# Kernel tuning notes

Hardware: AMD Instinct MI355X
Metric: run time of the kernel (lower is better)

Reference implementation:

```python
import jax, jax.numpy as jnp
import numpy as np

THRESHOLD = 0.35
NEGPOS = 7
VAR0, VAR1 = 0.1, 0.2


def point_form(boxes):
    # (cx,cy,w,h) -> (x1,y1,x2,y2)
    return jnp.concatenate([boxes[:, :2] - boxes[:, 2:] / 2,
                            boxes[:, :2] + boxes[:, 2:] / 2], axis=1)


def jaccard(box_a, box_b):
    # box_a: [T,4], box_b: [P,4] in point form -> IoU [T,P]
    max_xy = jnp.minimum(box_a[:, None, 2:], box_b[None, :, 2:])
    min_xy = jnp.maximum(box_a[:, None, :2], box_b[None, :, :2])
    wh = jnp.clip(max_xy - min_xy, 0.0)
    inter = wh[..., 0] * wh[..., 1]
    area_a = ((box_a[:, 2] - box_a[:, 0]) * (box_a[:, 3] - box_a[:, 1]))[:, None]
    area_b = ((box_b[:, 2] - box_b[:, 0]) * (box_b[:, 3] - box_b[:, 1]))[None, :]
    return inter / (area_a + area_b - inter)


def encode(matched, priors):
    # matched: [P,4] point form, priors: [P,4] center form
    g_cxcy = ((matched[:, :2] + matched[:, 2:]) / 2 - priors[:, :2]) / (VAR0 * priors[:, 2:])
    g_wh = jnp.log((matched[:, 2:] - matched[:, :2]) / priors[:, 2:]) / VAR1
    return jnp.concatenate([g_cxcy, g_wh], axis=1)


def encode_landm(matched, priors):
    m = matched.reshape(-1, 5, 2)                       # [P,5,2]
    g = (m - priors[:, None, :2]) / (VAR0 * priors[:, None, 2:])
    return g.reshape(-1, 10)


def match_one(truths, labels, landms, priors):
    # truths [T,4], labels [T], landms [T,10], priors [P,4]
    overlaps = jaccard(truths, point_form(priors))       # [T,P]
    best_prior_idx = jnp.argmax(overlaps, axis=1)        # [T]
    best_truth_overlap = overlaps.max(axis=0)            # [P]
    best_truth_idx = jnp.argmax(overlaps, axis=0)        # [P]
    best_truth_overlap = best_truth_overlap.at[best_prior_idx].set(2.0)
    def body(j, bti):
        return bti.at[best_prior_idx[j]].set(j)
    best_truth_idx = jax.lax.fori_loop(0, truths.shape[0], body, best_truth_idx)
    conf = jnp.where(best_truth_overlap < THRESHOLD, 0.0, labels[best_truth_idx])
    loc = encode(truths[best_truth_idx], priors)
    landm = encode_landm(landms[best_truth_idx], priors)
    return loc, conf, landm


def smooth_l1(p, t):
    d = jnp.abs(p - t)
    return jnp.where(d < 1.0, 0.5 * d * d, d - 0.5)


def reference(loc_data, conf_data, landm_data, priors, targets):
    num, num_priors, _ = loc_data.shape
    truths = targets[:, :, :4]
    landms = targets[:, :, 4:14]
    labels = targets[:, :, 14]
    loc_t, conf_f, landm_t = jax.vmap(match_one, in_axes=(0, 0, 0, None))(
        truths, labels, landms, priors)
    conf_t = conf_f.astype(jnp.int32)                    # [num, P]

    poslands = conf_t > 0
    loss_landm = jnp.sum(smooth_l1(landm_data, landm_t) * poslands[..., None])

    pos = conf_t != 0
    loss_l = jnp.sum(smooth_l1(loc_data, loc_t) * pos[..., None])

    conf_t = jnp.where(pos, 1, conf_t)
    # per-prior CE: logsumexp - logit[target]
    ce = jax.nn.logsumexp(conf_data, axis=-1) - \
        jnp.take_along_axis(conf_data, conf_t[..., None], axis=-1)[..., 0]

    # hard negative mining: rank negatives by CE, keep top negpos*num_pos
    loss_rank = jnp.where(pos, 0.0, ce)
    loss_idx = jnp.argsort(-loss_rank, axis=1)
    idx_rank = jnp.argsort(loss_idx, axis=1)
    num_pos = pos.sum(axis=1)
    num_neg = jnp.clip(NEGPOS * num_pos, 0, num_priors - 1)
    neg = idx_rank < num_neg[:, None]

    sel = pos | neg
    loss_c = jnp.sum(ce * sel)

    N = jnp.maximum(num_pos.sum().astype(loc_data.dtype), 1.0)
    N1 = jnp.maximum(poslands.sum().astype(loc_data.dtype), 1.0)
    return loss_l / N, loss_c / N, loss_landm / N1


def setup_inputs() -> dict:
    key = jax.random.key(0)
    ks = jax.random.split(key, 8)
    N, T, P = 16, 48, 65536
    loc_data = jax.random.normal(ks[0], (N, P, 4), dtype=jnp.float32) * 0.1
    conf_data = jax.random.normal(ks[1], (N, P, 2), dtype=jnp.float32)
    landm_data = jax.random.normal(ks[2], (N, P, 10), dtype=jnp.float32) * 0.1
    # priors in (cx,cy,w,h), w,h > 0
    pc = jax.random.uniform(ks[3], (P, 2), minval=0.05, maxval=0.95)
    pwh = jax.random.uniform(ks[4], (P, 2), minval=0.04, maxval=0.3)
    priors = jnp.concatenate([pc, pwh], axis=1).astype(jnp.float32)
    # GT boxes: valid point-form (x1<x2, y1<y2)
    tc = jax.random.uniform(ks[5], (N, T, 2), minval=0.1, maxval=0.9)
    twh = jax.random.uniform(ks[6], (N, T, 2), minval=0.05, maxval=0.3)
    boxes = jnp.concatenate([tc - twh / 2, tc + twh / 2], axis=-1)
    lm = jax.random.uniform(ks[7], (N, T, 10))
    labels = jnp.ones((N, T, 1))
    targets = jnp.concatenate([boxes, lm, labels], axis=-1).astype(jnp.float32)
    return {"loc_data": loc_data, "conf_data": conf_data,
            "landm_data": landm_data, "priors": priors, "targets": targets}
```

## Files before the change

kernel.cpp:

```cpp
#include <hip/hip_runtime.h>

#define NP 65536
#define NT 48
#define TH 0.35f
#define PPT 2
#define KC_BX 128
#define NCHUNK 16
#define NCPY 4

#define PERCHUNK_OFF 0
#define HISTC_OFF    98304
#define HISTS_OFF    622592
#define NEGSUM_OFF   1146880
#define PART_OFF     1147136
#define HIST_DWORDS  262144

__device__ __forceinline__ float sml1(float d) {
    float a = fabsf(d);
    return a < 1.f ? 0.5f * a * a : a - 0.5f;
}

__global__ __launch_bounds__(256) void kA(const float* __restrict__ priors,
                                          const float* __restrict__ targets,
                                          unsigned long long* __restrict__ perchunk,
                                          unsigned int* __restrict__ histz) {
    const int chunk = blockIdx.x, tg = blockIdx.y, b = blockIdx.z;
    {
        int flat = (b * 6 + tg) * NCHUNK + chunk;
        int base = flat * 171 + (int)threadIdx.x;
        if (threadIdx.x < 171 && base < HIST_DWORDS) histz[base] = 0u;
    }
    const float* tb = targets + ((size_t)b * NT + tg * 8) * 15;
    float tx1[8], ty1[8], tx2[8], ty2[8], ta[8];
#pragma unroll
    for (int j = 0; j < 8; j++) {
        tx1[j] = tb[j * 15 + 0]; ty1[j] = tb[j * 15 + 1];
        tx2[j] = tb[j * 15 + 2]; ty2[j] = tb[j * 15 + 3];
        ta[j] = (tx2[j] - tx1[j]) * (ty2[j] - ty1[j]);
    }
    const int pbase = chunk * 4096;
    float bi[8], bs[8]; unsigned int bp_[8];
#pragma unroll
    for (int j = 0; j < 8; j++) { bi[j] = 0.f; bs[j] = 1.f; bp_[j] = pbase + threadIdx.x; }
    const float4* P4 = reinterpret_cast<const float4*>(priors);
    for (int i = threadIdx.x; i < 4096; i += 256) {
        const int p = pbase + i;
        const float4 q = P4[p];
        const float px1 = q.x - q.z * 0.5f, py1 = q.y - q.w * 0.5f;
        const float px2 = q.x + q.z * 0.5f, py2 = q.y + q.w * 0.5f;
        const float areaB = (px2 - px1) * (py2 - py1);
#pragma unroll
        for (int j = 0; j < 8; j++) {
            float w = fminf(tx2[j], px2) - fmaxf(tx1[j], px1);
            float h = fminf(ty2[j], py2) - fmaxf(ty1[j], py1);
            w = fmaxf(w, 0.f); h = fmaxf(h, 0.f);
            float inter = w * h;
            float S = ta[j] + areaB;
            if (inter * bs[j] > bi[j] * S) { bi[j] = inter; bs[j] = S; bp_[j] = (unsigned int)p; }
        }
    }
    __shared__ unsigned long long red[4][8];
    const int lane = threadIdx.x & 63, w = threadIdx.x >> 6;
#pragma unroll
    for (int j = 0; j < 8; j++) {
        float bu = bs[j] - bi[j];
        float iou = bi[j] / bu;
        unsigned long long key =
            ((unsigned long long)__float_as_uint(iou) << 32) | (unsigned long long)(~bp_[j]);
        for (int s = 32; s > 0; s >>= 1) {
            unsigned long long o = __shfl_down(key, s, 64);
            if (o > key) key = o;
        }
        if (lane == 0) red[w][j] = key;
    }
    __syncthreads();
    if (threadIdx.x < 8) {
        unsigned long long m = red[0][threadIdx.x];
#pragma unroll
        for (int i = 1; i < 4; i++) { unsigned long long o = red[i][threadIdx.x]; if (o > m) m = o; }
        perchunk[((size_t)b * NT + tg * 8 + threadIdx.x) * NCHUNK + chunk] = m;
    }
}

__global__ __launch_bounds__(256) void kC(
    const float* __restrict__ loc_data, const float* __restrict__ conf_data,
    const float* __restrict__ landm_data, const float* __restrict__ priors,
    const float* __restrict__ targets, const unsigned long long* __restrict__ perchunk,
    unsigned int* __restrict__ hist_cnt, float* __restrict__ hist_sum,
    float* __restrict__ part) {
    const int b = blockIdx.y;
    const int bx = blockIdx.x;
    const int p0 = (bx * 256 + threadIdx.x) * PPT;
    const int blockBase = bx * 256 * PPT;

    __shared__ float4 tbox[NT];
    __shared__ float tlab[NT];
    __shared__ float tlm[NT][10];
    __shared__ unsigned int hcnt[2048];
    __shared__ float hsum[2048];
    __shared__ int ccnt;
    __shared__ int clp[NT], clt[NT];

    if (threadIdx.x == 0) ccnt = 0;
#pragma unroll
    for (int i = 0; i < 8; i++) { hcnt[threadIdx.x + i * 256] = 0; hsum[threadIdx.x + i * 256] = 0.f; }
    for (int i = threadIdx.x; i < NT * 15; i += 256) {
        int t = i / 15, f = i - t * 15;
        float v = targets[((size_t)b * NT + t) * 15 + f];
        if (f < 4) reinterpret_cast<float*>(&tbox[t])[f] = v;
        else if (f < 14) tlm[t][f - 4] = v;
        else tlab[t] = v;
    }
    __syncthreads();
    if (threadIdx.x < NT) {
        const unsigned long long* pk = perchunk + ((size_t)b * NT + threadIdx.x) * NCHUNK;
        unsigned long long m = pk[0];
#pragma unroll
        for (int c = 1; c < NCHUNK; c++) { unsigned long long o = pk[c]; if (o > m) m = o; }
        int cp = (int)(~(unsigned int)(m & 0xFFFFFFFFull));
        if ((unsigned int)(cp - blockBase) < (unsigned int)(256 * PPT)) {
            int idx = atomicAdd(&ccnt, 1);
            clp[idx] = cp; clt[idx] = threadIdx.x;
        }
    }
    __syncthreads();

    float px1[PPT], py1[PPT], px2[PPT], py2[PPT], aB[PPT];
    float bi[PPT], bs[PPT]; int bt[PPT];
#pragma unroll
    for (int j = 0; j < PPT; j++) {
        float4 q = reinterpret_cast<const float4*>(priors)[p0 + j];
        px1[j] = q.x - q.z * 0.5f; py1[j] = q.y - q.w * 0.5f;
        px2[j] = q.x + q.z * 0.5f; py2[j] = q.y + q.w * 0.5f;
        aB[j] = (px2[j] - px1[j]) * (py2[j] - py1[j]);
        bi[j] = 0.f; bs[j] = 1.f; bt[j] = 0;
    }

    for (int t = 0; t < NT; t++) {
        float4 tb = tbox[t];
        float ta = (tb.z - tb.x) * (tb.w - tb.y);
#pragma unroll
        for (int j = 0; j < PPT; j++) {
            float w = fminf(tb.z, px2[j]) - fmaxf(tb.x, px1[j]);
            float h = fminf(tb.w, py2[j]) - fmaxf(tb.y, py1[j]);
            w = fmaxf(w, 0.f); h = fmaxf(h, 0.f);
            float inter = w * h;
            float S = ta + aB[j];
            if (inter * bs[j] > bi[j] * S) { bi[j] = inter; bs[j] = S; bt[j] = t; }
        }
    }
    bool clf[PPT];
#pragma unroll
    for (int j = 0; j < PPT; j++) clf[j] = false;
    for (int i = 0; i < ccnt; i++) {
        int cp = clp[i], ct = clt[i];
        unsigned int d = (unsigned int)(cp - p0);
        if (d < PPT) {
#pragma unroll
            for (int j = 0; j < PPT; j++) {
                if (d == (unsigned int)j) {
                    bt[j] = clf[j] ? max(bt[j], ct) : ct;
                    clf[j] = true;
                }
            }
        }
    }

    const float4 cf = reinterpret_cast<const float4*>(conf_data)[((size_t)b * NP + p0) >> 1];
    float cx[PPT] = {cf.x, cf.z};
    float cy[PPT] = {cf.y, cf.w};

    float sl = 0.f, slm = 0.f, cep = 0.f;
    int cp_ = 0, cpl_ = 0;
#pragma unroll
    for (int j = 0; j < PPT; j++) {
        const int btj = bt[j];
        const bool over = clf[j] || (bi[j] >= TH * (bs[j] - bi[j]));
        const int confi = over ? (int)tlab[btj] : 0;
        const bool pos = (confi != 0);
        const bool posl = (confi > 0);
        float m = fmaxf(cx[j], cy[j]);
        float lse = m + __logf(__expf(cx[j] - m) + __expf(cy[j] - m));
        float ce = lse - (pos ? cy[j] : cx[j]);
        float lr = pos ? 0.f : fmaxf(ce, 0.f);
        unsigned int bin = __float_as_uint(lr) >> 20;
        atomicAdd(&hcnt[bin], 1u);
        if (lr != 0.f) atomicAdd(&hsum[bin], lr);
        if (pos) {
            cep += ce; cp_++;
            float4 q = reinterpret_cast<const float4*>(priors)[p0 + j];
            float4 tb = tbox[btj];
            float izi = 1.f / (0.1f * q.z), iwi = 1.f / (0.1f * q.w);
            float gcx = ((tb.x + tb.z) * 0.5f - q.x) * izi;
            float gcy = ((tb.y + tb.w) * 0.5f - q.y) * iwi;
            float gw = __logf((tb.z - tb.x) / q.z) * 5.f;
            float gh = __logf((tb.w - tb.y) / q.w) * 5.f;
            float4 ld = reinterpret_cast<const float4*>(loc_data)[(size_t)b * NP + p0 + j];
            sl += sml1(ld.x - gcx) + sml1(ld.y - gcy) + sml1(ld.z - gw) + sml1(ld.w - gh);
            if (posl) {
                cpl_++;
                const float* lmd = landm_data + ((size_t)b * NP + p0 + j) * 10;
#pragma unroll
                for (int i = 0; i < 5; i++) {
                    float gx = (tlm[btj][2 * i] - q.x) * izi;
                    float gy = (tlm[btj][2 * i + 1] - q.y) * iwi;
                    slm += sml1(lmd[2 * i] - gx) + sml1(lmd[2 * i + 1] - gy);
                }
            }
        }
    }

    for (int s = 32; s > 0; s >>= 1) {
        sl += __shfl_down(sl, s, 64);
        slm += __shfl_down(slm, s, 64);
        cep += __shfl_down(cep, s, 64);
        cp_ += __shfl_down(cp_, s, 64);
        cpl_ += __shfl_down(cpl_, s, 64);
    }
    __shared__ float rf[12];
    __shared__ int ri[8];
    const int lane = threadIdx.x & 63, w = threadIdx.x >> 6;
    if (lane == 0) { rf[w] = sl; rf[4 + w] = slm; rf[8 + w] = cep; ri[w] = cp_; ri[4 + w] = cpl_; }
    __syncthreads();
    if (threadIdx.x == 0) {
        float a = 0, bb = 0, c = 0; int d = 0, e = 0;
        for (int i = 0; i < 4; i++) { a += rf[i]; bb += rf[4 + i]; c += rf[8 + i]; d += ri[i]; e += ri[4 + i]; }
        float* pp = part + ((size_t)b * KC_BX + bx) * 8;
        pp[0] = a; pp[1] = bb; pp[2] = c; pp[3] = (float)d; pp[4] = (float)e;
    }
    {
        const unsigned int cidx = ((unsigned int)(bx & (NCPY - 1)) * 16 + b) << 11;
        unsigned int* gc = hist_cnt + cidx;
        float* gs = hist_sum + cidx;
#pragma unroll
        for (int i = 0; i < 8; i++) {
            unsigned int c = hcnt[threadIdx.x + i * 256];
            if (c) atomicAdd(&gc[threadIdx.x + i * 256], c);
            float s = hsum[threadIdx.x + i * 256];
            if (s != 0.f) atomicAdd(&gs[threadIdx.x + i * 256], s);
        }
    }
}

__global__ __launch_bounds__(256) void kF(const unsigned int* __restrict__ hist_cnt,
                                          const float* __restrict__ hist_sum,
                                          const float* __restrict__ part,
                                          float* __restrict__ negsum) {
    const int b = blockIdx.x;
    __shared__ float pk[2];
    __shared__ unsigned int shc[2048];
    __shared__ float shs[2048];
    __shared__ unsigned int ps[256];
    __shared__ int sbin;
    __shared__ unsigned int sacc;
    __shared__ float wsum[4];

    {
        float v = (threadIdx.x < KC_BX)
                      ? part[((size_t)b * KC_BX + threadIdx.x) * 8 + 3] : 0.f;
        for (int s = 32; s > 0; s >>= 1) v += __shfl_down(v, s, 64);
        if ((threadIdx.x & 63) == 0 && threadIdx.x < 128) pk[threadIdx.x >> 6] = v;
    }
    for (int off = 0; off < 2048; off += 256) {
        unsigned int c = 0; float s = 0.f;
#pragma unroll
        for (int cp = 0; cp < NCPY; cp++) {
            unsigned int idx = (((unsigned int)cp * 16 + b) << 11) + off + threadIdx.x;
            c += hist_cnt[idx];
            s += hist_sum[idx];
        }
        shc[off + threadIdx.x] = c;
        shs[off + threadIdx.x] = s;
    }
    __syncthreads();
    int k = 7 * (int)(pk[0] + pk[1] + 0.5f);
    if (k > NP - 1) k = NP - 1;
    if (k <= 0) { if (threadIdx.x == 0) negsum[b] = 0.f; return; }

    {
        unsigned int s = 0;
#pragma unroll
        for (int i = 0; i < 8; i++) s += shc[threadIdx.x * 8 + i];
        ps[threadIdx.x] = s;
    }
    __syncthreads();
    if (threadIdx.x == 0) {
        unsigned int kk = (unsigned int)k, acc = 0; int g = 255;
        for (; g > 0; --g) { unsigned int pg = ps[g]; if (acc + pg >= kk) break; acc += pg; }
        int bin = g * 8;
        for (int i = 7; i >= 0; --i) {
            unsigned int c = shc[g * 8 + i];
            if (acc + c >= kk) { bin = g * 8 + i; break; }
            acc += c;
        }
        sbin = bin; sacc = acc;
    }
    __syncthreads();
    const int b1 = sbin;
    float sum = 0.f;
    for (int i = threadIdx.x; i < 2048; i += 256)
        if (i > b1) sum += shs[i];
    for (int s = 32; s > 0; s >>= 1) sum += __shfl_down(sum, s, 64);
    const int lane = threadIdx.x & 63, w = threadIdx.x >> 6;
    if (lane == 0) wsum[w] = sum;
    __syncthreads();
    if (threadIdx.x == 0) {
        float tot = wsum[0] + wsum[1] + wsum[2] + wsum[3];
        unsigned int k2 = (unsigned int)k - sacc;
        tot += (float)k2 * __uint_as_float(((unsigned int)b1 << 20) | 0x80000u);
        negsum[b] = tot;
    }
}

__global__ __launch_bounds__(1024) void kE(const float* __restrict__ part,
                                           const float* __restrict__ negsum,
                                           float* __restrict__ out) {
    float sl = 0.f, slm = 0.f, cep = 0.f, cp = 0.f, cpl = 0.f;
#pragma unroll
    for (int r = 0; r < 2; r++) {
        const float* pp = part + ((size_t)threadIdx.x + r * 1024) * 8;
        sl += pp[0]; slm += pp[1]; cep += pp[2]; cp += pp[3]; cpl += pp[4];
    }
    float ns = (threadIdx.x < 16) ? negsum[threadIdx.x] : 0.f;
    for (int s = 32; s > 0; s >>= 1) {
        sl += __shfl_down(sl, s, 64);
        slm += __shfl_down(slm, s, 64);
        cep += __shfl_down(cep, s, 64);
        cp += __shfl_down(cp, s, 64);
        cpl += __shfl_down(cpl, s, 64);
        ns += __shfl_down(ns, s, 64);
    }
    __shared__ float r_[16][6];
    const int lane = threadIdx.x & 63, w = threadIdx.x >> 6;
    if (lane == 0) {
        r_[w][0] = sl; r_[w][1] = slm; r_[w][2] = cep;
        r_[w][3] = cp; r_[w][4] = cpl; r_[w][5] = ns;
    }
    __syncthreads();
    if (threadIdx.x == 0) {
        float a = 0, bb = 0, c = 0, d = 0, e = 0, n = 0;
        for (int i = 0; i < 16; i++) {
            a += r_[i][0]; bb += r_[i][1]; c += r_[i][2];
            d += r_[i][3]; e += r_[i][4]; n += r_[i][5];
        }
        float N = fmaxf(d, 1.f);
        float N1 = fmaxf(e, 1.f);
        out[0] = a / N;
        out[1] = (c + n) / N;
        out[2] = bb / N1;
    }
}

extern "C" void kernel_launch(void* const* d_in, const int* in_sizes, int n_in,
                              void* d_out, int out_size, void* d_ws, size_t ws_size,
                              hipStream_t stream) {
    const float* loc_data = (const float*)d_in[0];
    const float* conf_data = (const float*)d_in[1];
    const float* landm_data = (const float*)d_in[2];
    const float* priors = (const float*)d_in[3];
    const float* targets = (const float*)d_in[4];
    float* out = (float*)d_out;
    char* ws = (char*)d_ws;
    unsigned long long* perchunk = (unsigned long long*)(ws + PERCHUNK_OFF);
    unsigned int* hist_cnt = (unsigned int*)(ws + HISTC_OFF);
    float* hist_sum = (float*)(ws + HISTS_OFF);
    float* negsum = (float*)(ws + NEGSUM_OFF);
    float* part = (float*)(ws + PART_OFF);

    kA<<<dim3(NCHUNK, 6, 16), 256, 0, stream>>>(priors, targets, perchunk, hist_cnt);
    kC<<<dim3(KC_BX, 16), 256, 0, stream>>>(loc_data, conf_data, landm_data, priors, targets,
                                            perchunk, hist_cnt, hist_sum, part);
    kF<<<16, 256, 0, stream>>>(hist_cnt, hist_sum, part, negsum);
    kE<<<1, 1024, 0, stream>>>(part, negsum, out);
}
```

Before: 175.1 us.

## Fuse final reduction into kF via atomics, halve histogram copies, precompute target areas

```diff
diff --git a/kernel.cpp b/kernel.cpp
--- a/kernel.cpp
+++ b/kernel.cpp
@@ -6,14 +6,15 @@
 #define PPT 2
 #define KC_BX 128
 #define NCHUNK 16
-#define NCPY 4
+#define NCPY 2
 
 #define PERCHUNK_OFF 0
-#define HISTC_OFF    98304
-#define HISTS_OFF    622592
-#define NEGSUM_OFF   1146880
-#define PART_OFF     1147136
-#define HIST_DWORDS  262144
+#define ACCF_OFF     98304
+#define DONE_OFF     98336
+#define HISTC_OFF    98368
+#define HISTS_OFF    360512
+#define PART_OFF     622656
+#define ZERO_DWORDS  131088
 
 __device__ __forceinline__ float sml1(float d) {
     float a = fabsf(d);
@@ -23,12 +24,12 @@
 __global__ __launch_bounds__(256) void kA(const float* __restrict__ priors,
                                           const float* __restrict__ targets,
                                           unsigned long long* __restrict__ perchunk,
-                                          unsigned int* __restrict__ histz) {
+                                          unsigned int* __restrict__ zbase) {
     const int chunk = blockIdx.x, tg = blockIdx.y, b = blockIdx.z;
     {
         int flat = (b * 6 + tg) * NCHUNK + chunk;
-        int base = flat * 171 + (int)threadIdx.x;
-        if (threadIdx.x < 171 && base < HIST_DWORDS) histz[base] = 0u;
+        int base = flat * 96 + (int)threadIdx.x;
+        if (threadIdx.x < 96 && base < ZERO_DWORDS) zbase[base] = 0u;
     }
     const float* tb = targets + ((size_t)b * NT + tg * 8) * 15;
     float tx1[8], ty1[8], tx2[8], ty2[8], ta[8];
@@ -94,6 +95,7 @@
     const int blockBase = bx * 256 * PPT;
 
     __shared__ float4 tbox[NT];
+    __shared__ float tarea[NT];
     __shared__ float tlab[NT];
     __shared__ float tlm[NT][10];
     __shared__ unsigned int hcnt[2048];
@@ -102,8 +104,11 @@
     __shared__ int clp[NT], clt[NT];
 
     if (threadIdx.x == 0) ccnt = 0;
-#pragma unroll
-    for (int i = 0; i < 8; i++) { hcnt[threadIdx.x + i * 256] = 0; hsum[threadIdx.x + i * 256] = 0.f; }
+    {
+        const int hb = threadIdx.x * 8;
+#pragma unroll
+        for (int i = 0; i < 8; i++) { hcnt[hb + i] = 0; hsum[hb + i] = 0.f; }
+    }
     for (int i = threadIdx.x; i < NT * 15; i += 256) {
         int t = i / 15, f = i - t * 15;
         float v = targets[((size_t)b * NT + t) * 15 + f];
@@ -113,6 +118,8 @@
     }
     __syncthreads();
     if (threadIdx.x < NT) {
+        float4 tb = tbox[threadIdx.x];
+        tarea[threadIdx.x] = (tb.z - tb.x) * (tb.w - tb.y);
         const unsigned long long* pk = perchunk + ((size_t)b * NT + threadIdx.x) * NCHUNK;
         unsigned long long m = pk[0];
 #pragma unroll
@@ -136,9 +143,10 @@
         bi[j] = 0.f; bs[j] = 1.f; bt[j] = 0;
     }
 
+#pragma unroll 4
     for (int t = 0; t < NT; t++) {
         float4 tb = tbox[t];
-        float ta = (tb.z - tb.x) * (tb.w - tb.y);
+        float ta = tarea[t];
 #pragma unroll
         for (int j = 0; j < PPT; j++) {
             float w = fminf(tb.z, px2[j]) - fmaxf(tb.x, px1[j]);
@@ -180,7 +188,7 @@
         const bool pos = (confi != 0);
         const bool posl = (confi > 0);
         float m = fmaxf(cx[j], cy[j]);
-        float lse = m + __logf(__expf(cx[j] - m) + __expf(cy[j] - m));
+        float lse = m + __logf(1.f + __expf(-fabsf(cx[j] - cy[j])));
         float ce = lse - (pos ? cy[j] : cx[j]);
         float lr = pos ? 0.f : fmaxf(ce, 0.f);
         unsigned int bin = __float_as_uint(lr) >> 20;
@@ -245,9 +253,11 @@
 __global__ __launch_bounds__(256) void kF(const unsigned int* __restrict__ hist_cnt,
                                           const float* __restrict__ hist_sum,
                                           const float* __restrict__ part,
-                                          float* __restrict__ negsum) {
+                                          float* __restrict__ accf,
+                                          unsigned int* __restrict__ done_cnt,
+                                          float* __restrict__ out) {
     const int b = blockIdx.x;
-    __shared__ float pk[2];
+    __shared__ float rsum[2][5];
     __shared__ unsigned int shc[2048];
     __shared__ float shs[2048];
     __shared__ unsigned int ps[256];
@@ -256,10 +266,22 @@
     __shared__ float wsum[4];
 
     {
-        float v = (threadIdx.x < KC_BX)
-                      ? part[((size_t)b * KC_BX + threadIdx.x) * 8 + 3] : 0.f;
-        for (int s = 32; s > 0; s >>= 1) v += __shfl_down(v, s, 64);
-        if ((threadIdx.x & 63) == 0 && threadIdx.x < 128) pk[threadIdx.x >> 6] = v;
+        float v0 = 0, v1 = 0, v2 = 0, v3 = 0, v4 = 0;
+        if (threadIdx.x < KC_BX) {
+            const float* pp = part + ((size_t)b * KC_BX + threadIdx.x) * 8;
+            v0 = pp[0]; v1 = pp[1]; v2 = pp[2]; v3 = pp[3]; v4 = pp[4];
+        }
+        for (int s = 32; s > 0; s >>= 1) {
+            v0 += __shfl_down(v0, s, 64);
+            v1 += __shfl_down(v1, s, 64);
+            v2 += __shfl_down(v2, s, 64);
+            v3 += __shfl_down(v3, s, 64);
+            v4 += __shfl_down(v4, s, 64);
+        }
+        if ((threadIdx.x & 63) == 0 && threadIdx.x < 128) {
+            int w = threadIdx.x >> 6;
+            rsum[w][0] = v0; rsum[w][1] = v1; rsum[w][2] = v2; rsum[w][3] = v3; rsum[w][4] = v4;
+        }
     }
     for (int off = 0; off < 2048; off += 256) {
         unsigned int c = 0; float s = 0.f;
@@ -273,9 +295,9 @@
         shs[off + threadIdx.x] = s;
     }
     __syncthreads();
-    int k = 7 * (int)(pk[0] + pk[1] + 0.5f);
+    int k = 7 * (int)(rsum[0][3] + rsum[1][3] + 0.5f);
     if (k > NP - 1) k = NP - 1;
-    if (k <= 0) { if (threadIdx.x == 0) negsum[b] = 0.f; return; }
+    if (k < 0) k = 0;
 
     {
         unsigned int s = 0;
@@ -307,47 +329,29 @@
     if (threadIdx.x == 0) {
         float tot = wsum[0] + wsum[1] + wsum[2] + wsum[3];
         unsigned int k2 = (unsigned int)k - sacc;
-        tot += (float)k2 * __uint_as_float(((unsigned int)b1 << 20) | 0x80000u);
-        negsum[b] = tot;
-    }
-}
-
-__global__ __launch_bounds__(1024) void kE(const float* __restrict__ part,
-                                           const float* __restrict__ negsum,
-                                           float* __restrict__ out) {
-    float sl = 0.f, slm = 0.f, cep = 0.f, cp = 0.f, cpl = 0.f;
-#pragma unroll
-    for (int r = 0; r < 2; r++) {
-        const float* pp = part + ((size_t)threadIdx.x + r * 1024) * 8;
-        sl += pp[0]; slm += pp[1]; cep += pp[2]; cp += pp[3]; cpl += pp[4];
-    }
-    float ns = (threadIdx.x < 16) ? negsum[threadIdx.x] : 0.f;
-    for (int s = 32; s > 0; s >>= 1) {
-        sl += __shfl_down(sl, s, 64);
-        slm += __shfl_down(slm, s, 64);
-        cep += __shfl_down(cep, s, 64);
-        cp += __shfl_down(cp, s, 64);
-        cpl += __shfl_down(cpl, s, 64);
-        ns += __shfl_down(ns, s, 64);
-    }
-    __shared__ float r_[16][6];
-    const int lane = threadIdx.x & 63, w = threadIdx.x >> 6;
-    if (lane == 0) {
-        r_[w][0] = sl; r_[w][1] = slm; r_[w][2] = cep;
-        r_[w][3] = cp; r_[w][4] = cpl; r_[w][5] = ns;
-    }
-    __syncthreads();
-    if (threadIdx.x == 0) {
-        float a = 0, bb = 0, c = 0, d = 0, e = 0, n = 0;
-        for (int i = 0; i < 16; i++) {
-            a += r_[i][0]; bb += r_[i][1]; c += r_[i][2];
-            d += r_[i][3]; e += r_[i][4]; n += r_[i][5];
-        }
-        float N = fmaxf(d, 1.f);
-        float N1 = fmaxf(e, 1.f);
-        out[0] = a / N;
-        out[1] = (c + n) / N;
-        out[2] = bb / N1;
+        if (k > 0) tot += (float)k2 * __uint_as_float(((unsigned int)b1 << 20) | 0x80000u);
+        atomicAdd(&accf[0], rsum[0][0] + rsum[1][0]);
+        atomicAdd(&accf[1], rsum[0][1] + rsum[1][1]);
+        atomicAdd(&accf[2], rsum[0][2] + rsum[1][2]);
+        atomicAdd(&accf[3], rsum[0][3] + rsum[1][3]);
+        atomicAdd(&accf[4], rsum[0][4] + rsum[1][4]);
+        atomicAdd(&accf[5], tot);
+        __threadfence();
+        unsigned int prev = atomicAdd(done_cnt, 1u);
+        if (prev == 15u) {
+            __threadfence();
+            float a  = atomicAdd(&accf[0], 0.f);
+            float bb = atomicAdd(&accf[1], 0.f);
+            float c  = atomicAdd(&accf[2], 0.f);
+            float d  = atomicAdd(&accf[3], 0.f);
+            float e  = atomicAdd(&accf[4], 0.f);
+            float n  = atomicAdd(&accf[5], 0.f);
+            float N = fmaxf(d, 1.f);
+            float N1 = fmaxf(e, 1.f);
+            out[0] = a / N;
+            out[1] = (c + n) / N;
+            out[2] = bb / N1;
+        }
     }
 }
 
@@ -362,14 +366,15 @@
     float* out = (float*)d_out;
     char* ws = (char*)d_ws;
     unsigned long long* perchunk = (unsigned long long*)(ws + PERCHUNK_OFF);
+    float* accf = (float*)(ws + ACCF_OFF);
+    unsigned int* done_cnt = (unsigned int*)(ws + DONE_OFF);
     unsigned int* hist_cnt = (unsigned int*)(ws + HISTC_OFF);
     float* hist_sum = (float*)(ws + HISTS_OFF);
-    float* negsum = (float*)(ws + NEGSUM_OFF);
     float* part = (float*)(ws + PART_OFF);
 
-    kA<<<dim3(NCHUNK, 6, 16), 256, 0, stream>>>(priors, targets, perchunk, hist_cnt);
+    kA<<<dim3(NCHUNK, 6, 16), 256, 0, stream>>>(priors, targets, perchunk,
+                                                (unsigned int*)(ws + ACCF_OFF));
     kC<<<dim3(KC_BX, 16), 256, 0, stream>>>(loc_data, conf_data, landm_data, priors, targets,
                                             perchunk, hist_cnt, hist_sum, part);
-    kF<<<16, 256, 0, stream>>>(hist_cnt, hist_sum, part, negsum);
-    kE<<<1, 1024, 0, stream>>>(part, negsum, out);
-}
+    kF<<<16, 256, 0, stream>>>(hist_cnt, hist_sum, part, accf, done_cnt, out);
+}
```

Measured after the change: 164.7 us. -5.9%, faster.
